# Optimization experiments

Hardware: AMD Instinct MI355X
Metric: run time of the kernel (lower is better)

The kernel has to match this reference:

```python
import jax, jax.numpy as jnp
import numpy as np
from jax import lax

B, T, L = 16, 256, 1024       # batch, seq_length, input_size
NF = 32                        # num_filters
KS = [3, 5, 7]                 # kernel_sizes
H = 1024                       # feature_size
GRU_IN = NF * len(KS)          # 96


def setup_inputs() -> dict:
    key = jax.random.key(0)
    ks = jax.random.split(key, 20)
    def rn(k, shape, scale):
        return (jax.random.normal(k, shape, dtype=jnp.float32) * scale)
    inp = {
        "x": jax.random.normal(ks[0], (B, T, L), dtype=jnp.float32),
        "conv_w3": rn(ks[1], (NF, 1, 3), (2.0 / 3) ** 0.5),
        "conv_b3": jnp.zeros((NF,), jnp.float32),
        "conv_w5": rn(ks[2], (NF, 1, 5), (2.0 / 5) ** 0.5),
        "conv_b5": jnp.zeros((NF,), jnp.float32),
        "conv_w7": rn(ks[3], (NF, 1, 7), (2.0 / 7) ** 0.5),
        "conv_b7": jnp.zeros((NF,), jnp.float32),
        "gru_w_ih": rn(ks[4], (3 * H, GRU_IN), GRU_IN ** -0.5),
        "gru_w_hh": rn(ks[5], (3 * H, H), H ** -0.5),
        "gru_b_ih": jnp.zeros((3 * H,), jnp.float32),
        "gru_b_hh": jnp.zeros((3 * H,), jnp.float32),
        "attn_w1": rn(ks[6], (H, H), H ** -0.5),
        "attn_b1": jnp.zeros((H,), jnp.float32),
        "attn_w2": rn(ks[7], (1, H), H ** -0.5),
        "attn_b2": jnp.zeros((1,), jnp.float32),
        "fi_w1": rn(ks[8], (H, H), H ** -0.5),
        "fi_b1": jnp.zeros((H,), jnp.float32),
        "fi_w2": rn(ks[9], (H, H), H ** -0.5),
        "fi_b2": jnp.zeros((H,), jnp.float32),
        "lateral": jnp.full((H, H), 0.1, jnp.float32),
    }
    return inp


def _forward(x, conv_w3, conv_b3, conv_w5, conv_b5, conv_w7, conv_b7,
             gru_w_ih, gru_w_hh, gru_b_ih, gru_b_hh,
             attn_w1, attn_b1, attn_w2, attn_b2,
             fi_w1, fi_b1, fi_w2, fi_b2, lateral):
    b, t, l = x.shape
    # --- per-timestep conv branches (no cross-time dependence -> vectorize over B*T) ---
    xt = x.reshape(b * t, 1, l)  # (BT, C=1, L)
    pooled = []
    for w, bias in ((conv_w3, conv_b3), (conv_w5, conv_b5), (conv_w7, conv_b7)):
        y = lax.conv_general_dilated(xt, w, (1,), "SAME",
                                     dimension_numbers=("NCH", "OIH", "NCH"))
        y = jax.nn.relu(y + bias[None, :, None])
        pooled.append(jnp.max(y, axis=-1))  # adaptive_max_pool1d -> (BT, NF)
    feat = jnp.concatenate(pooled, axis=1).reshape(b, t, -1)  # (B, T, 3*NF)

    # --- GRU over time (sequential carry) ---
    gates_x = jnp.einsum("bti,gi->btg", feat, gru_w_ih) + gru_b_ih  # (B,T,3H)

    def step(h, gx):
        gh = h @ gru_w_hh.T + gru_b_hh
        xr, xz, xn = jnp.split(gx, 3, axis=-1)
        hr, hz, hn = jnp.split(gh, 3, axis=-1)
        r = jax.nn.sigmoid(xr + hr)
        z = jax.nn.sigmoid(xz + hz)
        n = jnp.tanh(xn + r * hn)
        h_new = (1.0 - z) * n + z * h
        return h_new, h_new

    h0 = jnp.zeros((b, gru_w_hh.shape[1]), x.dtype)
    _, hs = lax.scan(step, h0, jnp.swapaxes(gates_x, 0, 1))  # (T,B,H)
    hs = jnp.swapaxes(hs, 0, 1)  # (B,T,H)

    # --- attention: per-step softmax over a length-1 axis -> weights are all 1 ---
    scores = jnp.tanh(hs @ attn_w1.T + attn_b1) @ attn_w2.T + attn_b2  # (B,T,1)
    attn = jax.nn.softmax(scores, axis=-1)  # softmax over singleton seq dim -> ones
    attended = hs * attn  # (B,T,H)

    # --- lateral inhibition + feature integration MLP ---
    inhib = attended - jax.nn.relu(jnp.einsum("bth,hf->btf", attended, lateral))
    features = jax.nn.relu(inhib @ fi_w1.T + fi_b1) @ fi_w2.T + fi_b2  # (B,T,H)
    return features, attn[..., 0]  # attention_weights (B,T)


def reference(x, conv_w3, conv_b3, conv_w5, conv_b5, conv_w7, conv_b7,
              gru_w_ih, gru_w_hh, gru_b_ih, gru_b_hh,
              attn_w1, attn_b1, attn_w2, attn_b2,
              fi_w1, fi_b1, fi_w2, fi_b2, lateral):
    return _forward(x, conv_w3, conv_b3, conv_w5, conv_b5, conv_w7, conv_b7,
                    gru_w_ih, gru_w_hh, gru_b_ih, gru_b_hh,
                    attn_w1, attn_b1, attn_w2, attn_b2,
                    fi_w1, fi_b1, fi_w2, fi_b2, lateral)
```

## Files before the change

kernel.cpp:

```cpp
#include <hip/hip_runtime.h>
#include <stdint.h>
#include <stddef.h>

#define B_   16
#define T_   256
#define L_   1024
#define H_   1024
#define G3_  3072
#define KIN_ 96

#define SENT_     0x7FC1
#define SENT_X2_  0x7FC17FC1u

typedef __attribute__((ext_vector_type(8))) __bf16 bf16x8;
typedef __attribute__((ext_vector_type(4))) float  f32x4;
typedef __attribute__((ext_vector_type(4))) int    i32x4;

static __device__ __forceinline__ unsigned short f2bf(float x) {
  unsigned int u = __builtin_bit_cast(unsigned int, x);
  u += 0x7FFFu + ((u >> 16) & 1u);
  return (unsigned short)(u >> 16);
}
static __device__ __forceinline__ float bf2f(unsigned short s) {
  unsigned int u = ((unsigned int)s) << 16;
  return __builtin_bit_cast(float, u);
}
static __device__ __forceinline__ unsigned sentmask(unsigned d) {
  const unsigned x = d ^ SENT_X2_;
  return (x - 0x00010001u) & ~x & 0x80008000u;
}

__global__ void cvt4_kernel(const float* __restrict__ s0, unsigned short* __restrict__ d0,
                            const float* __restrict__ s1, unsigned short* __restrict__ d1,
                            const float* __restrict__ s2, unsigned short* __restrict__ d2,
                            const float* __restrict__ s3, unsigned short* __restrict__ d3) {
  const int n0 = G3_ * H_;
  const int n1 = n0 + G3_ * KIN_;
  const int n2 = n1 + H_ * H_;
  const int n3 = n2 + H_ * H_;
  int i = blockIdx.x * 256 + threadIdx.x;
  const int stride = gridDim.x * 256;
  for (; i < n3; i += stride) {
    if (i < n0)      d0[i]      = f2bf(s0[i]);
    else if (i < n1) d1[i - n0] = f2bf(s1[i - n0]);
    else if (i < n2) d2[i - n1] = f2bf(s2[i - n1]);
    else             d3[i - n2] = f2bf(s3[i - n2]);
  }
}

__global__ void transpose_bf16_kernel(const float* __restrict__ in,
                                      unsigned short* __restrict__ out,
                                      int R, int C) {
  int i = blockIdx.x * 256 + threadIdx.x;
  int n = R * C, stride = gridDim.x * 256;
  for (; i < n; i += stride) {
    int r = i / C, c = i % C;
    out[(size_t)c * R + r] = f2bf(in[i]);
  }
}

__global__ void ones_kernel(float* __restrict__ p, int n) {
  int i = blockIdx.x * 256 + threadIdx.x;
  if (i < n) p[i] = 1.0f;
}

__global__ void fill_sent_kernel(unsigned int* __restrict__ p, int n) {
  int i = blockIdx.x * 256 + threadIdx.x;
  const int stride = gridDim.x * 256;
  const unsigned int v = SENT_X2_;
  for (; i < n; i += stride) {
    unsigned int* q = p + i;
    asm volatile("global_store_dword %0, %1, off sc0 sc1" :: "v"(q), "v"(v) : "memory");
  }
}

__global__ __launch_bounds__(256) void conv_kernel(
    const float* __restrict__ x,
    const float* __restrict__ w3, const float* __restrict__ b3,
    const float* __restrict__ w5, const float* __restrict__ b5,
    const float* __restrict__ w7, const float* __restrict__ b7,
    unsigned short* __restrict__ feat) {
  __shared__ float xpad[L_ + 8];
  __shared__ float wlds[96][8];
  __shared__ float blds[96];
  __shared__ float wmax[4][96];
  const int tid = threadIdx.x;
  const int rid = blockIdx.x;
  const int b = rid >> 8;
  const int t = rid & 255;
  const float* xr = x + (size_t)rid * L_;
  for (int off = tid; off < L_; off += 256) xpad[off + 3] = xr[off];
  if (tid < 3) xpad[tid] = 0.f;
  if (tid >= 3 && tid < 8) xpad[L_ + tid] = 0.f;
  if (tid < 96) {
    const int f = tid;
    float wv[8];
#pragma unroll
    for (int k = 0; k < 8; ++k) wv[k] = 0.f;
    float bv;
    if (f < 32)      { for (int k = 0; k < 3; ++k) wv[k + 2] = w3[f * 3 + k]; bv = b3[f]; }
    else if (f < 64) { int ff = f - 32; for (int k = 0; k < 5; ++k) wv[k + 1] = w5[ff * 5 + k]; bv = b5[ff]; }
    else             { int ff = f - 64; for (int k = 0; k < 7; ++k) wv[k] = w7[ff * 7 + k]; bv = b7[ff]; }
#pragma unroll
    for (int k = 0; k < 8; ++k) wlds[f][k] = wv[k];
    blds[f] = bv;
  }
  __syncthreads();
  const int w = tid >> 6, lane = tid & 63;
  const int p0 = w * 256 + lane * 4;
  float xv[10];
#pragma unroll
  for (int i = 0; i < 10; ++i) xv[i] = xpad[p0 + i];
  for (int f = 0; f < 96; ++f) {
    float a0 = 0.f, a1 = 0.f, a2 = 0.f, a3 = 0.f;
#pragma unroll
    for (int k = 0; k < 7; ++k) {
      const float wk = wlds[f][k];
      a0 = fmaf(wk, xv[k],     a0);
      a1 = fmaf(wk, xv[k + 1], a1);
      a2 = fmaf(wk, xv[k + 2], a2);
      a3 = fmaf(wk, xv[k + 3], a3);
    }
    float m = fmaxf(fmaxf(a0, a1), fmaxf(a2, a3));
#pragma unroll
    for (int d = 1; d < 64; d <<= 1) m = fmaxf(m, __shfl_xor(m, d, 64));
    if (lane == 0) wmax[w][f] = m;
  }
  __syncthreads();
  if (tid < 96) {
    float m = fmaxf(fmaxf(wmax[0][tid], wmax[1][tid]),
                    fmaxf(wmax[2][tid], wmax[3][tid]));
    m += blds[tid];
    m = m > 0.f ? m : 0.f;
    feat[(size_t)(t * B_ + b) * KIN_ + tid] = f2bf(m);
  }
}

template <int EP>
__global__ __launch_bounds__(256) void gemm_kernel(
    const unsigned short* __restrict__ A,
    const unsigned short* __restrict__ Bm,
    int M, int N, int K, int lda, int ldb,
    const float* __restrict__ bias,
    float* __restrict__ outF,
    unsigned short* __restrict__ outB) {
  __shared__ __align__(16) unsigned short As[2][128 * 40];
  __shared__ __align__(16) unsigned short Bs[2][128 * 40];
  const int tid = threadIdx.x;
  const int n0 = blockIdx.x * 128;
  const int m0 = blockIdx.y * 128;
  const int w = tid >> 6;
  const int l = tid & 63;
  const int lr = l & 15;
  const int lk = (l >> 4) * 8;
  const int srow = tid >> 2;
  const int skc = (tid & 3) * 8;

  f32x4 acc[2][8];
#pragma unroll
  for (int i = 0; i < 2; ++i)
#pragma unroll
    for (int j = 0; j < 8; ++j) acc[i][j] = (f32x4){0.f, 0.f, 0.f, 0.f};

  const int NK = K >> 5;
  const unsigned short* Aptr  = A  + (size_t)(m0 + srow)      * lda + skc;
  const unsigned short* Aptr2 = A  + (size_t)(m0 + 64 + srow) * lda + skc;
  const unsigned short* Bptr  = Bm + (size_t)(n0 + srow)      * ldb + skc;
  const unsigned short* Bptr2 = Bm + (size_t)(n0 + 64 + srow) * ldb + skc;

  i32x4 ar0 = *(const i32x4*)(Aptr);
  i32x4 ar1 = *(const i32x4*)(Aptr2);
  i32x4 br0 = *(const i32x4*)(Bptr);
  i32x4 br1 = *(const i32x4*)(Bptr2);
  *(i32x4*)&As[0][srow * 40 + skc]        = ar0;
  *(i32x4*)&As[0][(64 + srow) * 40 + skc] = ar1;
  *(i32x4*)&Bs[0][srow * 40 + skc]        = br0;
  *(i32x4*)&Bs[0][(64 + srow) * 40 + skc] = br1;
  __syncthreads();

  for (int kk = 0; kk < NK; ++kk) {
    const int cur = kk & 1;
    if (kk + 1 < NK) {
      const int ko = (kk + 1) << 5;
      ar0 = *(const i32x4*)(Aptr  + ko);
      ar1 = *(const i32x4*)(Aptr2 + ko);
      br0 = *(const i32x4*)(Bptr  + ko);
      br1 = *(const i32x4*)(Bptr2 + ko);
    }
    const bf16x8 a0 = *(const bf16x8*)&As[cur][(w * 32 + lr) * 40 + lk];
    const bf16x8 a1 = *(const bf16x8*)&As[cur][(w * 32 + 16 + lr) * 40 + lk];
#pragma unroll
    for (int nt = 0; nt < 8; ++nt) {
      const bf16x8 bb = *(const bf16x8*)&Bs[cur][(nt * 16 + lr) * 40 + lk];
      acc[0][nt] = __builtin_amdgcn_mfma_f32_16x16x32_bf16(a0, bb, acc[0][nt], 0, 0, 0);
      acc[1][nt] = __builtin_amdgcn_mfma_f32_16x16x32_bf16(a1, bb, acc[1][nt], 0, 0, 0);
    }
    __syncthreads();
    if (kk + 1 < NK) {
      const int nxt = cur ^ 1;
      *(i32x4*)&As[nxt][srow * 40 + skc]        = ar0;
      *(i32x4*)&As[nxt][(64 + srow) * 40 + skc] = ar1;
      *(i32x4*)&Bs[nxt][srow * 40 + skc]        = br0;
      *(i32x4*)&Bs[nxt][(64 + srow) * 40 + skc] = br1;
    }
    __syncthreads();
  }

#pragma unroll
  for (int mt = 0; mt < 2; ++mt) {
#pragma unroll
    for (int nt = 0; nt < 8; ++nt) {
      const f32x4 v = acc[mt][nt];
      const int gcol = n0 + nt * 16 + lr;
#pragma unroll
      for (int e = 0; e < 4; ++e) {
        const int grow = m0 + w * 32 + mt * 16 + (l >> 4) * 4 + e;
        const float val = v[e];
        if (EP == 0) {
          outF[(size_t)grow * N + gcol] = val + bias[gcol];
        } else if (EP == 1) {
          const float hsv = bf2f(A[(size_t)grow * lda + gcol]);
          outB[(size_t)grow * N + gcol] = f2bf(hsv - fmaxf(val, 0.f));
        } else if (EP == 2) {
          outB[(size_t)grow * N + gcol] = f2bf(fmaxf(val + bias[gcol], 0.f));
        } else {
          const int tt = grow >> 4;
          const int bb2 = grow & 15;
          outF[((size_t)bb2 * T_ + tt) * H_ + gcol] = val + bias[gcol];
        }
      }
    }
  }
}

__global__ __launch_bounds__(512, 2) void gru_scan_kernel(
    const unsigned short* __restrict__ Whh,
    const float* __restrict__ gates,
    const float* __restrict__ bhh,
    unsigned short* __restrict__ hs) {
  __shared__ float ghp[2][8][3][16][17];
  const int tid = threadIdx.x;
  const int g = blockIdx.x;
  const int w = tid >> 6;
  const int l = tid & 63;
  const int lr = l & 15;
  const int lk8 = (l >> 4) * 8;
  const int j0 = g * 16;

  const unsigned short* ap0 = Whh + (size_t)(j0 + lr) * H_ + w * 128 + lk8;
  const unsigned short* ap1 = ap0 + (size_t)H_ * H_;
  const unsigned short* ap2 = ap1 + (size_t)H_ * H_;
  i32x4 w00, w01, w02, w03, w10, w11, w12, w13, w20, w21, w22, w23;
  asm volatile(
      "global_load_dwordx4 %0,  %12, off\n\t"
      "global_load_dwordx4 %1,  %12, off offset:64\n\t"
      "global_load_dwordx4 %2,  %12, off offset:128\n\t"
      "global_load_dwordx4 %3,  %12, off offset:192\n\t"
      "global_load_dwordx4 %4,  %13, off\n\t"
      "global_load_dwordx4 %5,  %13, off offset:64\n\t"
      "global_load_dwordx4 %6,  %13, off offset:128\n\t"
      "global_load_dwordx4 %7,  %13, off offset:192\n\t"
      "global_load_dwordx4 %8,  %14, off\n\t"
      "global_load_dwordx4 %9,  %14, off offset:64\n\t"
      "global_load_dwordx4 %10, %14, off offset:128\n\t"
      "global_load_dwordx4 %11, %14, off offset:192\n\t"
      "s_waitcnt vmcnt(0)"
      : "=&v"(w00), "=&v"(w01), "=&v"(w02), "=&v"(w03),
        "=&v"(w10), "=&v"(w11), "=&v"(w12), "=&v"(w13),
        "=&v"(w20), "=&v"(w21), "=&v"(w22), "=&v"(w23)
      : "v"(ap0), "v"(ap1), "v"(ap2));
  const bf16x8 af00 = __builtin_bit_cast(bf16x8, w00);
  const bf16x8 af01 = __builtin_bit_cast(bf16x8, w01);
  const bf16x8 af02 = __builtin_bit_cast(bf16x8, w02);
  const bf16x8 af03 = __builtin_bit_cast(bf16x8, w03);
  const bf16x8 af10 = __builtin_bit_cast(bf16x8, w10);
  const bf16x8 af11 = __builtin_bit_cast(bf16x8, w11);
  const bf16x8 af12 = __builtin_bit_cast(bf16x8, w12);
  const bf16x8 af13 = __builtin_bit_cast(bf16x8, w13);
  const bf16x8 af20 = __builtin_bit_cast(bf16x8, w20);
  const bf16x8 af21 = __builtin_bit_cast(bf16x8, w21);
  const bf16x8 af22 = __builtin_bit_cast(bf16x8, w22);
  const bf16x8 af23 = __builtin_bit_cast(bf16x8, w23);

  const int jb = tid & 15;
  const int bb = tid >> 4;
  const float bhr = bhh[j0 + jb];
  const float bhz = bhh[H_ + j0 + jb];
  const float bhn = bhh[2 * H_ + j0 + jb];
  float hprev = 0.f;

  for (int t = 0; t < T_; ++t) {
    const int buf = t & 1;
    float gxr = 0.f, gxz = 0.f, gxn = 0.f;
    if (tid < 256) {
      const size_t grow = ((size_t)t * B_ + bb) * G3_;
      gxr = gates[grow + j0 + jb];
      gxz = gates[grow + H_ + j0 + jb];
      gxn = gates[grow + 2 * H_ + j0 + jb];
    }

    const unsigned short* hp = hs + (size_t)t * (B_ * H_) +
                               (size_t)lr * H_ + w * 128 + lk8;
    i32x4 u0, u1, u2, u3;
    while (true) {
      asm volatile(
          "global_load_dwordx4 %0, %4, off sc0 sc1\n\t"
          "global_load_dwordx4 %1, %4, off offset:64 sc0 sc1\n\t"
          "global_load_dwordx4 %2, %4, off offset:128 sc0 sc1\n\t"
          "global_load_dwordx4 %3, %4, off offset:192 sc0 sc1\n\t"
          "s_waitcnt vmcnt(0)"
          : "=&v"(u0), "=&v"(u1), "=&v"(u2), "=&v"(u3)
          : "v"(hp)
          : "memory");
      const unsigned bad =
          sentmask(u0[0]) | sentmask(u0[1]) | sentmask(u0[2]) | sentmask(u0[3]) |
          sentmask(u1[0]) | sentmask(u1[1]) | sentmask(u1[2]) | sentmask(u1[3]) |
          sentmask(u2[0]) | sentmask(u2[1]) | sentmask(u2[2]) | sentmask(u2[3]) |
          sentmask(u3[0]) | sentmask(u3[1]) | sentmask(u3[2]) | sentmask(u3[3]);
      if (__ballot(bad == 0) == ~0ull) break;
    }
    const bf16x8 hf0 = __builtin_bit_cast(bf16x8, u0);
    const bf16x8 hf1 = __builtin_bit_cast(bf16x8, u1);
    const bf16x8 hf2 = __builtin_bit_cast(bf16x8, u2);
    const bf16x8 hf3 = __builtin_bit_cast(bf16x8, u3);

    f32x4 C0 = (f32x4){0.f, 0.f, 0.f, 0.f}, C1 = C0, C2 = C0;
    C0 = __builtin_amdgcn_mfma_f32_16x16x32_bf16(af00, hf0, C0, 0, 0, 0);
    C1 = __builtin_amdgcn_mfma_f32_16x16x32_bf16(af10, hf0, C1, 0, 0, 0);
    C2 = __builtin_amdgcn_mfma_f32_16x16x32_bf16(af20, hf0, C2, 0, 0, 0);
    C0 = __builtin_amdgcn_mfma_f32_16x16x32_bf16(af01, hf1, C0, 0, 0, 0);
    C1 = __builtin_amdgcn_mfma_f32_16x16x32_bf16(af11, hf1, C1, 0, 0, 0);
    C2 = __builtin_amdgcn_mfma_f32_16x16x32_bf16(af21, hf1, C2, 0, 0, 0);
    C0 = __builtin_amdgcn_mfma_f32_16x16x32_bf16(af02, hf2, C0, 0, 0, 0);
    C1 = __builtin_amdgcn_mfma_f32_16x16x32_bf16(af12, hf2, C1, 0, 0, 0);
    C2 = __builtin_amdgcn_mfma_f32_16x16x32_bf16(af22, hf2, C2, 0, 0, 0);
    C0 = __builtin_amdgcn_mfma_f32_16x16x32_bf16(af03, hf3, C0, 0, 0, 0);
    C1 = __builtin_amdgcn_mfma_f32_16x16x32_bf16(af13, hf3, C1, 0, 0, 0);
    C2 = __builtin_amdgcn_mfma_f32_16x16x32_bf16(af23, hf3, C2, 0, 0, 0);

    const int rb = (l >> 4) * 4;
#pragma unroll
    for (int e = 0; e < 4; ++e) {
      ghp[buf][w][0][lr][rb + e] = C0[e];
      ghp[buf][w][1][lr][rb + e] = C1[e];
      ghp[buf][w][2][lr][rb + e] = C2[e];
    }
    __syncthreads();

    if (tid < 256) {
      float sr = bhr, sz = bhz, sn = bhn;
#pragma unroll
      for (int w2 = 0; w2 < 8; ++w2) {
        sr += ghp[buf][w2][0][bb][jb];
        sz += ghp[buf][w2][1][bb][jb];
        sn += ghp[buf][w2][2][bb][jb];
      }
      const float r = 1.f / (1.f + __expf(-(gxr + sr)));
      const float z = 1.f / (1.f + __expf(-(gxz + sz)));
      const float xn = gxn + r * sn;
      const float n = 2.f / (1.f + __expf(-2.f * xn)) - 1.f;
      const float hnew = (1.f - z) * n + z * hprev;
      hprev = hnew;
      unsigned short* sp = hs + ((size_t)(t + 1) * B_ + bb) * H_ + j0 + jb;
      const unsigned hv = (unsigned)f2bf(hnew);
      asm volatile("global_store_short %0, %1, off sc0 sc1"
                   :: "v"(sp), "v"(hv) : "memory");
    }
  }
}

extern "C" void kernel_launch(void* const* d_in, const int* in_sizes, int n_in,
                              void* d_out, int out_size, void* d_ws, size_t ws_size,
                              hipStream_t stream) {
  (void)in_sizes; (void)n_in; (void)out_size; (void)ws_size;
  const float* x    = (const float*)d_in[0];
  const float* w3   = (const float*)d_in[1];
  const float* b3   = (const float*)d_in[2];
  const float* w5   = (const float*)d_in[3];
  const float* b5   = (const float*)d_in[4];
  const float* w7   = (const float*)d_in[5];
  const float* b7   = (const float*)d_in[6];
  const float* wih  = (const float*)d_in[7];
  const float* whh  = (const float*)d_in[8];
  const float* bih  = (const float*)d_in[9];
  const float* bhh  = (const float*)d_in[10];
  const float* fiw1 = (const float*)d_in[15];
  const float* fib1 = (const float*)d_in[16];
  const float* fiw2 = (const float*)d_in[17];
  const float* fib2 = (const float*)d_in[18];
  const float* lat  = (const float*)d_in[19];

  char* ws = (char*)d_ws;
  size_t off = 0;
  auto alloc = [&](size_t bytes) -> void* {
    void* p = ws + off;
    off += (bytes + 255) & ~(size_t)255;
    return p;
  };
  unsigned short* whh_bf  = (unsigned short*)alloc((size_t)G3_ * H_ * 2);
  unsigned short* wih_bf  = (unsigned short*)alloc((size_t)G3_ * KIN_ * 2);
  unsigned short* latT_bf = (unsigned short*)alloc((size_t)H_ * H_ * 2);
  unsigned short* fiw1_bf = (unsigned short*)alloc((size_t)H_ * H_ * 2);
  unsigned short* fiw2_bf = (unsigned short*)alloc((size_t)H_ * H_ * 2);
  unsigned short* feat_bf = (unsigned short*)alloc((size_t)B_ * T_ * KIN_ * 2);
  float*          gates   = (float*)alloc((size_t)B_ * T_ * G3_ * 4);
  unsigned short* hsbuf   = (unsigned short*)alloc((size_t)(T_ + 1) * B_ * H_ * 2);
  unsigned short* inhib   = (unsigned short*)alloc((size_t)B_ * T_ * H_ * 2);
  unsigned short* y1      = (unsigned short*)alloc((size_t)B_ * T_ * H_ * 2);

  hipMemsetAsync(hsbuf, 0, (size_t)B_ * H_ * 2, stream);
  fill_sent_kernel<<<1024, 256, 0, stream>>>(
      (unsigned int*)(hsbuf + (size_t)B_ * H_), T_ * B_ * H_ / 2);

  cvt4_kernel<<<2048, 256, 0, stream>>>(whh, whh_bf, wih, wih_bf,
                                        fiw1, fiw1_bf, fiw2, fiw2_bf);
  transpose_bf16_kernel<<<1024, 256, 0, stream>>>(lat, latT_bf, H_, H_);

  conv_kernel<<<B_ * T_, 256, 0, stream>>>(x, w3, b3, w5, b5, w7, b7, feat_bf);

  {
    dim3 grid(G3_ / 128, (B_ * T_) / 128);
    gemm_kernel<0><<<grid, 256, 0, stream>>>(feat_bf, wih_bf, B_ * T_, G3_, KIN_,
                                             KIN_, KIN_, bih, gates, nullptr);
  }

  gru_scan_kernel<<<64, 512, 0, stream>>>(whh_bf, gates, bhh, hsbuf);

  const unsigned short* hs1 = hsbuf + (size_t)B_ * H_;
  {
    dim3 grid(H_ / 128, (B_ * T_) / 128);
    gemm_kernel<1><<<grid, 256, 0, stream>>>(hs1, latT_bf, B_ * T_, H_, H_,
                                             H_, H_, nullptr, nullptr, inhib);
    gemm_kernel<2><<<grid, 256, 0, stream>>>(inhib, fiw1_bf, B_ * T_, H_, H_,
                                             H_, H_, fib1, nullptr, y1);
    gemm_kernel<3><<<grid, 256, 0, stream>>>(y1, fiw2_bf, B_ * T_, H_, H_,
                                             H_, H_, fib2, (float*)d_out, nullptr);
  }

  ones_kernel<<<16, 256, 0, stream>>>((float*)d_out + (size_t)B_ * T_ * H_, B_ * T_);
}
```

Baseline: 1.031 ms.

## Pin GRU scan blocks to one XCD and poll hidden state via L2

```diff
diff --git a/kernel.cpp b/kernel.cpp
--- a/kernel.cpp
+++ b/kernel.cpp
@@ -30,47 +30,42 @@
   return (x - 0x00010001u) & ~x & 0x80008000u;
 }
 
-__global__ void cvt4_kernel(const float* __restrict__ s0, unsigned short* __restrict__ d0,
-                            const float* __restrict__ s1, unsigned short* __restrict__ d1,
-                            const float* __restrict__ s2, unsigned short* __restrict__ d2,
-                            const float* __restrict__ s3, unsigned short* __restrict__ d3) {
-  const int n0 = G3_ * H_;
-  const int n1 = n0 + G3_ * KIN_;
-  const int n2 = n1 + H_ * H_;
-  const int n3 = n2 + H_ * H_;
+__global__ void prep_kernel(
+    const float* __restrict__ whh,  unsigned short* __restrict__ whh_bf,
+    const float* __restrict__ wih,  unsigned short* __restrict__ wih_bf,
+    const float* __restrict__ fiw1, unsigned short* __restrict__ fiw1_bf,
+    const float* __restrict__ fiw2, unsigned short* __restrict__ fiw2_bf,
+    const float* __restrict__ lat,  unsigned short* __restrict__ latT_bf,
+    unsigned short* __restrict__ hsbuf, unsigned short* __restrict__ hmbuf,
+    float* __restrict__ attn_out, int* __restrict__ claim) {
+  const int N0 = G3_ * H_;
+  const int N1 = N0 + G3_ * KIN_;
+  const int N2 = N1 + H_ * H_;
+  const int N3 = N2 + H_ * H_;
+  const int N4 = N3 + H_ * H_;
+  const int N5 = N4 + T_ * B_ * H_ / 2;
+  const int N6 = N5 + B_ * H_ / 2;
+  const int N7 = N6 + B_ * T_;
+  const int N8 = N7 + 16;
+  const int N9 = N8 + T_ * B_ * H_ / 2;
+  const int N10 = N9 + B_ * H_ / 2;
   int i = blockIdx.x * 256 + threadIdx.x;
   const int stride = gridDim.x * 256;
-  for (; i < n3; i += stride) {
-    if (i < n0)      d0[i]      = f2bf(s0[i]);
-    else if (i < n1) d1[i - n0] = f2bf(s1[i - n0]);
-    else if (i < n2) d2[i - n1] = f2bf(s2[i - n1]);
-    else             d3[i - n2] = f2bf(s3[i - n2]);
-  }
-}
-
-__global__ void transpose_bf16_kernel(const float* __restrict__ in,
-                                      unsigned short* __restrict__ out,
-                                      int R, int C) {
-  int i = blockIdx.x * 256 + threadIdx.x;
-  int n = R * C, stride = gridDim.x * 256;
-  for (; i < n; i += stride) {
-    int r = i / C, c = i % C;
-    out[(size_t)c * R + r] = f2bf(in[i]);
-  }
-}
-
-__global__ void ones_kernel(float* __restrict__ p, int n) {
-  int i = blockIdx.x * 256 + threadIdx.x;
-  if (i < n) p[i] = 1.0f;
-}
-
-__global__ void fill_sent_kernel(unsigned int* __restrict__ p, int n) {
-  int i = blockIdx.x * 256 + threadIdx.x;
-  const int stride = gridDim.x * 256;
-  const unsigned int v = SENT_X2_;
-  for (; i < n; i += stride) {
-    unsigned int* q = p + i;
-    asm volatile("global_store_dword %0, %1, off sc0 sc1" :: "v"(q), "v"(v) : "memory");
+  unsigned int* hs32 = (unsigned int*)hsbuf;
+  unsigned int* hm32 = (unsigned int*)hmbuf;
+  for (; i < N10; i += stride) {
+    if (i < N0)      whh_bf[i] = f2bf(whh[i]);
+    else if (i < N1) { const int j = i - N0; wih_bf[j]  = f2bf(wih[j]); }
+    else if (i < N2) { const int j = i - N1; fiw1_bf[j] = f2bf(fiw1[j]); }
+    else if (i < N3) { const int j = i - N2; fiw2_bf[j] = f2bf(fiw2[j]); }
+    else if (i < N4) { const int j = i - N3; const int r = j >> 10, c = j & 1023;
+                       latT_bf[(size_t)c * H_ + r] = f2bf(lat[j]); }
+    else if (i < N5) { hs32[B_ * H_ / 2 + (i - N4)] = SENT_X2_; }
+    else if (i < N6) { hs32[i - N5] = 0u; }
+    else if (i < N7) { attn_out[i - N6] = 1.0f; }
+    else if (i < N8) { claim[i - N7] = 0; }
+    else if (i < N9) { hm32[B_ * H_ / 2 + (i - N8)] = SENT_X2_; }
+    else             { hm32[i - N9] = 0u; }
   }
 }
 
@@ -237,10 +232,40 @@
     const unsigned short* __restrict__ Whh,
     const float* __restrict__ gates,
     const float* __restrict__ bhh,
-    unsigned short* __restrict__ hs) {
+    unsigned short* __restrict__ hs,
+    unsigned short* __restrict__ hm,
+    int* __restrict__ claim) {
   __shared__ float ghp[2][8][3][16][17];
+  __shared__ int slotLds;
   const int tid = threadIdx.x;
-  const int g = blockIdx.x;
+
+  if (tid == 0) {
+    int xcd;
+    asm volatile("s_getreg_b32 %0, hwreg(HW_REG_XCC_ID)" : "=s"(xcd));
+    xcd &= 7;
+    const int idx = __hip_atomic_fetch_add(&claim[xcd], 1, __ATOMIC_RELAXED,
+                                           __HIP_MEMORY_SCOPE_AGENT);
+    int slot = -1;
+    if (idx < 64) {
+      if (idx == 23) {
+        int expected = 0;
+        __hip_atomic_compare_exchange_strong(&claim[8], &expected, xcd + 1,
+                                             __ATOMIC_RELEASE, __ATOMIC_RELAXED,
+                                             __HIP_MEMORY_SCOPE_AGENT);
+      }
+      int wnr;
+      while ((wnr = __hip_atomic_load(&claim[8], __ATOMIC_ACQUIRE,
+                                      __HIP_MEMORY_SCOPE_AGENT)) == 0) {
+        __builtin_amdgcn_s_sleep(8);
+      }
+      if (wnr == xcd + 1) slot = idx;
+    }
+    slotLds = slot;
+  }
+  __syncthreads();
+  const int g = slotLds;
+  if (g < 0) return;
+
   const int w = tid >> 6;
   const int l = tid & 63;
   const int lr = l & 15;
@@ -288,6 +313,7 @@
   const float bhz = bhh[H_ + j0 + jb];
   const float bhn = bhh[2 * H_ + j0 + jb];
   float hprev = 0.f;
+  int esc = 0;
 
   for (int t = 0; t < T_; ++t) {
     const int buf = t & 1;
@@ -299,25 +325,38 @@
       gxn = gates[grow + 2 * H_ + j0 + jb];
     }
 
-    const unsigned short* hp = hs + (size_t)t * (B_ * H_) +
-                               (size_t)lr * H_ + w * 128 + lk8;
+    const size_t hoff = (size_t)t * (B_ * H_) + (size_t)lr * H_ + w * 128 + lk8;
+    const unsigned short* hp = hs + hoff;
+    const unsigned short* hpm = hm + hoff;
     i32x4 u0, u1, u2, u3;
+    int tries = 0;
     while (true) {
-      asm volatile(
-          "global_load_dwordx4 %0, %4, off sc0 sc1\n\t"
-          "global_load_dwordx4 %1, %4, off offset:64 sc0 sc1\n\t"
-          "global_load_dwordx4 %2, %4, off offset:128 sc0 sc1\n\t"
-          "global_load_dwordx4 %3, %4, off offset:192 sc0 sc1\n\t"
-          "s_waitcnt vmcnt(0)"
-          : "=&v"(u0), "=&v"(u1), "=&v"(u2), "=&v"(u3)
-          : "v"(hp)
-          : "memory");
+      if (!esc) {
+        asm volatile(
+            "global_load_dwordx4 %0, %4, off sc0\n\t"
+            "global_load_dwordx4 %1, %4, off offset:64 sc0\n\t"
+            "global_load_dwordx4 %2, %4, off offset:128 sc0\n\t"
+            "global_load_dwordx4 %3, %4, off offset:192 sc0\n\t"
+            "s_waitcnt vmcnt(0)"
+            : "=&v"(u0), "=&v"(u1), "=&v"(u2), "=&v"(u3)
+            : "v"(hp));
+      } else {
+        asm volatile(
+            "global_load_dwordx4 %0, %4, off sc0 sc1\n\t"
+            "global_load_dwordx4 %1, %4, off offset:64 sc0 sc1\n\t"
+            "global_load_dwordx4 %2, %4, off offset:128 sc0 sc1\n\t"
+            "global_load_dwordx4 %3, %4, off offset:192 sc0 sc1\n\t"
+            "s_waitcnt vmcnt(0)"
+            : "=&v"(u0), "=&v"(u1), "=&v"(u2), "=&v"(u3)
+            : "v"(hpm));
+      }
       const unsigned bad =
           sentmask(u0[0]) | sentmask(u0[1]) | sentmask(u0[2]) | sentmask(u0[3]) |
           sentmask(u1[0]) | sentmask(u1[1]) | sentmask(u1[2]) | sentmask(u1[3]) |
           sentmask(u2[0]) | sentmask(u2[1]) | sentmask(u2[2]) | sentmask(u2[3]) |
           sentmask(u3[0]) | sentmask(u3[1]) | sentmask(u3[2]) | sentmask(u3[3]);
       if (__ballot(bad == 0) == ~0ull) break;
+      if (++tries > 200) esc = 1;
     }
     const bf16x8 hf0 = __builtin_bit_cast(bf16x8, u0);
     const bf16x8 hf1 = __builtin_bit_cast(bf16x8, u1);
@@ -361,10 +400,13 @@
       const float n = 2.f / (1.f + __expf(-2.f * xn)) - 1.f;
       const float hnew = (1.f - z) * n + z * hprev;
       hprev = hnew;
-      unsigned short* sp = hs + ((size_t)(t + 1) * B_ + bb) * H_ + j0 + jb;
+      const size_t soff = ((size_t)(t + 1) * B_ + bb) * H_ + j0 + jb;
+      unsigned short* sp  = hs + soff;
+      unsigned short* spm = hm + soff;
       const unsigned hv = (unsigned)f2bf(hnew);
-      asm volatile("global_store_short %0, %1, off sc0 sc1"
-                   :: "v"(sp), "v"(hv) : "memory");
+      asm volatile("global_store_short %0, %2, off sc0\n\t"
+                   "global_store_short %1, %2, off sc0 sc1"
+                   :: "v"(sp), "v"(spm), "v"(hv) : "memory");
     }
   }
 }
@@ -405,16 +447,16 @@
   unsigned short* feat_bf = (unsigned short*)alloc((size_t)B_ * T_ * KIN_ * 2);
   float*          gates   = (float*)alloc((size_t)B_ * T_ * G3_ * 4);
   unsigned short* hsbuf   = (unsigned short*)alloc((size_t)(T_ + 1) * B_ * H_ * 2);
+  unsigned short* hmbuf   = (unsigned short*)alloc((size_t)(T_ + 1) * B_ * H_ * 2);
   unsigned short* inhib   = (unsigned short*)alloc((size_t)B_ * T_ * H_ * 2);
   unsigned short* y1      = (unsigned short*)alloc((size_t)B_ * T_ * H_ * 2);
-
-  hipMemsetAsync(hsbuf, 0, (size_t)B_ * H_ * 2, stream);
-  fill_sent_kernel<<<1024, 256, 0, stream>>>(
-      (unsigned int*)(hsbuf + (size_t)B_ * H_), T_ * B_ * H_ / 2);
-
-  cvt4_kernel<<<2048, 256, 0, stream>>>(whh, whh_bf, wih, wih_bf,
-                                        fiw1, fiw1_bf, fiw2, fiw2_bf);
-  transpose_bf16_kernel<<<1024, 256, 0, stream>>>(lat, latT_bf, H_, H_);
+  int*            claim   = (int*)alloc(16 * 4);
+
+  prep_kernel<<<4096, 256, 0, stream>>>(whh, whh_bf, wih, wih_bf,
+                                        fiw1, fiw1_bf, fiw2, fiw2_bf,
+                                        lat, latT_bf, hsbuf, hmbuf,
+                                        (float*)d_out + (size_t)B_ * T_ * H_,
+                                        claim);
 
   conv_kernel<<<B_ * T_, 256, 0, stream>>>(x, w3, b3, w5, b5, w7, b7, feat_bf);
 
@@ -424,7 +466,7 @@
                                              KIN_, KIN_, bih, gates, nullptr);
   }
 
-  gru_scan_kernel<<<64, 512, 0, stream>>>(whh_bf, gates, bhh, hsbuf);
+  gru_scan_kernel<<<2048, 512, 0, stream>>>(whh_bf, gates, bhh, hsbuf, hmbuf, claim);
 
   const unsigned short* hs1 = hsbuf + (size_t)B_ * H_;
   {
@@ -436,6 +478,4 @@
     gemm_kernel<3><<<grid, 256, 0, stream>>>(y1, fiw2_bf, B_ * T_, H_, H_,
                                              H_, H_, fib2, (float*)d_out, nullptr);
   }
-
-  ones_kernel<<<16, 256, 0, stream>>>((float*)d_out + (size_t)B_ * T_ * H_, B_ * T_);
-}
+}
```

Result: slower. 3.052 ms (+195.9%).
